# Kernel tuning notes

Hardware: AMD Instinct MI355X
Metric: run time of the kernel (lower is better)

The kernel has to match this reference:

```python
import jax, jax.numpy as jnp
import numpy as np

IN_DIM, H, OUT_DIM = 64, 128, 64
B, T = 1024, 512
NEG_SLOPE = 0.01
LN_EPS = 1e-5


def _mlp_layer(x, W, b, g, beta):
    h = x @ W.T + b
    h = jnp.where(h > 0, h, NEG_SLOPE * h)  # LeakyReLU
    mu = h.mean(-1, keepdims=True)
    var = h.var(-1, keepdims=True)
    return g * (h - mu) / jnp.sqrt(var + LN_EPS) + beta


def setup_inputs() -> dict:
    key = jax.random.key(0)
    ks = jax.random.split(key, 16)
    s = 1.0 / np.sqrt(H)
    return {
        "x": jax.random.normal(ks[0], (B, T, IN_DIM), jnp.float32),
        "is_init": jax.random.randint(ks[1], (B, T, 1), 0, 2) > 0,
        "hx": jax.random.normal(ks[2], (B, H), jnp.float32),
        "W1": jax.random.uniform(ks[3], (H, IN_DIM), jnp.float32, -s, s),
        "b1": jnp.zeros((H,), jnp.float32),
        "g1": jnp.ones((H,), jnp.float32),
        "beta1": jnp.zeros((H,), jnp.float32),
        "W2": jax.random.uniform(ks[4], (H, H), jnp.float32, -s, s),
        "b2": jnp.zeros((H,), jnp.float32),
        "g2": jnp.ones((H,), jnp.float32),
        "beta2": jnp.zeros((H,), jnp.float32),
        "W_ih": jax.random.uniform(ks[5], (3 * H, H), jnp.float32, -s, s),
        "W_hh": jax.random.uniform(ks[6], (3 * H, H), jnp.float32, -s, s),
        "b_ih": jax.random.uniform(ks[7], (3 * H,), jnp.float32, -s, s),
        "b_hh": jax.random.uniform(ks[8], (3 * H,), jnp.float32, -s, s),
        "W_out": jax.random.uniform(ks[9], (OUT_DIM, H), jnp.float32, -s, s),
        "b_out": jnp.zeros((OUT_DIM,), jnp.float32),
    }


def reference(x, is_init, hx, W1, b1, g1, beta1, W2, b2, g2, beta2,
              W_ih, W_hh, b_ih, b_hh, W_out, b_out):
    # MLP: two (Linear -> LeakyReLU -> LayerNorm) layers, width 128
    h = _mlp_layer(x, W1, b1, g1, beta1)
    h = _mlp_layer(h, W2, b2, g2, beta2)

    # Precompute input-side gate preactivations for all timesteps: [B,T,3H]
    gates_x = h @ W_ih.T + b_ih
    gates_x_t = jnp.swapaxes(gates_x, 0, 1)      # [T,B,3H]
    init_t = jnp.swapaxes(is_init, 0, 1)         # [T,B,1]

    def step(h_prev, inp):
        gx, init = inp
        h_prev = jnp.where(init, 0.0, h_prev)    # reset-on-init
        gh = h_prev @ W_hh.T + b_hh
        xr, xz, xn = jnp.split(gx, 3, axis=-1)
        hr, hz, hn = jnp.split(gh, 3, axis=-1)
        r = jax.nn.sigmoid(xr + hr)
        z = jax.nn.sigmoid(xz + hz)
        n = jnp.tanh(xn + r * hn)
        h_new = (1.0 - z) * n + z * h_prev
        return h_new, h_new

    hx_final, ys = jax.lax.scan(step, hx, (gates_x_t, init_t))
    y = jnp.swapaxes(ys, 0, 1)                   # [B,T,H]
    out = y @ W_out.T + b_out                    # [B,T,OUT_DIM]
    return out, hx_final
```

## Files before the change

kernel.cpp:

```cpp
#include <hip/hip_runtime.h>
#include <hip/hip_bf16.h>

#define IN_DIM 64
#define H 128
#define G3 384
#define OUT_DIM 64
#define Bb 1024
#define Tt 512
#define NEG 0.01f
#define EPSLN 1e-5f

#define CHUNK 16
#define NTILE (Tt / CHUNK)

typedef __bf16 bf16_t;
typedef __bf16 bf16x8 __attribute__((ext_vector_type(8)));
typedef float f32x4 __attribute__((ext_vector_type(4)));

#define MFMA(a, b, c) __builtin_amdgcn_mfma_f32_16x16x32_bf16((a), (b), (c), 0, 0, 0)

#define WS_W1 0
#define WS_W2 8192
#define WS_WIH 24576
#define WS_WHH 73728
#define WS_WOUT 122880
#define WS_ELEMS 131072
#define WS_E_OFF 262144
#define WS_R_OFF (WS_E_OFF + 16777216)
#define WS_RA_OFF (WS_R_OFF + 131072)
#define WS_NEED (WS_RA_OFF + 131072)

#define HAS 136
#define GXS 392

__global__ void cvt_weights(const float* __restrict__ W1, const float* __restrict__ W2,
                            const float* __restrict__ Wih, const float* __restrict__ Whh,
                            const float* __restrict__ Wout, bf16_t* __restrict__ ws,
                            int* __restrict__ RA) {
    int i = blockIdx.x * 256 + threadIdx.x;
    float v;
    if (i < WS_W2) v = W1[i];
    else if (i < WS_WIH) v = W2[i - WS_W2];
    else if (i < WS_WHH) v = Wih[i - WS_WIH];
    else if (i < WS_WOUT) v = Whh[i - WS_WHH];
    else v = Wout[i - WS_WOUT];
    ws[i] = (bf16_t)v;
    if (i < Bb * NTILE) RA[i] = 0;
}

#define P1_GX 0
#define P1_HA 50176
#define P1_HPB 67584
#define P1_RED 76288
#define P1_MNR 78336
#define P1_INI 78848
#define P1_SMEM 79120
#define BPB1 4

__global__ void __launch_bounds__(256, 2) gru_pass1(
    const float* __restrict__ x, const int* __restrict__ is_init,
    const float* __restrict__ hx,
    const float* __restrict__ b1, const float* __restrict__ g1, const float* __restrict__ be1,
    const float* __restrict__ b2, const float* __restrict__ g2, const float* __restrict__ be2,
    const float* __restrict__ bih, const float* __restrict__ bhh,
    const float* __restrict__ bout,
    const bf16_t* __restrict__ wsb,
    float* __restrict__ E, int* __restrict__ R,
    float* __restrict__ out)
{
    extern __shared__ char smem[];
    bf16_t* GX  = (bf16_t*)(smem + P1_GX);
    bf16_t* HA  = (bf16_t*)(smem + P1_HA);
    bf16_t* HPB = (bf16_t*)(smem + P1_HPB);
    float*  RED = (float*) (smem + P1_RED);
    float*  MNR = (float*) (smem + P1_MNR);
    int*    INI = (int*)   (smem + P1_INI);

    const bf16_t* W1B  = wsb + WS_W1;
    const bf16_t* W2B  = wsb + WS_W2;
    const bf16_t* WihB = wsb + WS_WIH;
    const bf16_t* WhhB = wsb + WS_WHH;
    const bf16_t* WoB  = wsb + WS_WOUT;

    const int tid  = threadIdx.x;
    const int w    = tid >> 6;
    const int lane = tid & 63;
    const int ln   = lane & 15;
    const int quad = lane >> 4;
    const int b0   = blockIdx.x * BPB1;
    const int tile = blockIdx.y;
    const int t0   = tile * CHUNK;

    for (int i = tid; i < 2 * 16 * HAS; i += 256) HPB[i] = (bf16_t)0.f;
    __syncthreads();

    float hp[2] = {0.f, 0.f};
    if (tile == 0) {
        const int b = quad;
        int im = is_init[(size_t)(b0 + b) * Tt];
#pragma unroll
        for (int sub = 0; sub < 2; ++sub) {
            int j = w * 32 + sub * 16 + ln;
            float v = im ? 0.f : hx[(size_t)(b0 + b) * H + j];
            hp[sub] = v;
            HPB[b * 4 * HAS + j] = (bf16_t)v;
        }
    }
    float bh[3][2];
#pragma unroll
    for (int g = 0; g < 3; ++g)
#pragma unroll
        for (int sub = 0; sub < 2; ++sub)
            bh[g][sub] = bhh[g * H + w * 32 + sub * 16 + ln];

    bf16x8 whhf[6][4];
#pragma unroll
    for (int ntl = 0; ntl < 6; ++ntl) {
        int gate = ntl >> 1, sub = ntl & 1;
        int n = gate * H + w * 32 + sub * 16 + ln;
#pragma unroll
        for (int ks = 0; ks < 4; ++ks)
            whhf[ntl][ks] = *(const bf16x8*)(WhhB + (size_t)n * H + ks * 32 + quad * 8);
    }
    __syncthreads();

    f32x4 vs[BPB1][2];

    {
        bf16x8 w1f[2][2];
#pragma unroll
        for (int ntl = 0; ntl < 2; ++ntl) {
            int n = w * 32 + ntl * 16 + ln;
#pragma unroll
            for (int ks = 0; ks < 2; ++ks)
                w1f[ntl][ks] = *(const bf16x8*)(W1B + (size_t)n * IN_DIM + ks * 32 + quad * 8);
        }
#pragma unroll
        for (int mt = 0; mt < BPB1; ++mt) {
            const float* xr_ = x + ((size_t)(b0 + mt) * Tt + t0 + ln) * IN_DIM;
            bf16x8 a0, a1;
#pragma unroll
            for (int j = 0; j < 8; ++j) {
                a0[j] = (bf16_t)xr_[quad * 8 + j];
                a1[j] = (bf16_t)xr_[32 + quad * 8 + j];
            }
#pragma unroll
            for (int ntl = 0; ntl < 2; ++ntl) {
                f32x4 c = {0.f, 0.f, 0.f, 0.f};
                c = MFMA(a0, w1f[ntl][0], c);
                c = MFMA(a1, w1f[ntl][1], c);
                vs[mt][ntl] = c;
            }
        }
        float bv[2], gv[2], bev[2];
#pragma unroll
        for (int ntl = 0; ntl < 2; ++ntl) {
            int n = w * 32 + ntl * 16 + ln;
            bv[ntl] = b1[n]; gv[ntl] = g1[n]; bev[ntl] = be1[n];
        }
#pragma unroll
        for (int mt = 0; mt < BPB1; ++mt) {
#pragma unroll
            for (int reg = 0; reg < 4; ++reg) {
                float v0 = vs[mt][0][reg] + bv[0]; v0 = v0 > 0.f ? v0 : NEG * v0;
                float v1 = vs[mt][1][reg] + bv[1]; v1 = v1 > 0.f ? v1 : NEG * v1;
                vs[mt][0][reg] = v0; vs[mt][1][reg] = v1;
                float s = v0 + v1, q = v0 * v0 + v1 * v1;
#pragma unroll
                for (int d = 1; d < 16; d <<= 1) { s += __shfl_xor(s, d); q += __shfl_xor(q, d); }
                if (ln == 0) {
                    int rr = mt * 16 + quad * 4 + reg;
                    RED[rr * 8 + w] = s; RED[rr * 8 + 4 + w] = q;
                }
            }
        }
        __syncthreads();
        if (tid < 64) {
            float s = RED[tid * 8] + RED[tid * 8 + 1] + RED[tid * 8 + 2] + RED[tid * 8 + 3];
            float q = RED[tid * 8 + 4] + RED[tid * 8 + 5] + RED[tid * 8 + 6] + RED[tid * 8 + 7];
            float mean = s * (1.f / H);
            float var = q * (1.f / H) - mean * mean;
            MNR[tid * 2] = mean; MNR[tid * 2 + 1] = rsqrtf(var + EPSLN);
        }
        __syncthreads();
#pragma unroll
        for (int mt = 0; mt < BPB1; ++mt) {
#pragma unroll
            for (int reg = 0; reg < 4; ++reg) {
                int rr = mt * 16 + quad * 4 + reg;
                float mean = MNR[rr * 2], rstd = MNR[rr * 2 + 1];
#pragma unroll
                for (int ntl = 0; ntl < 2; ++ntl) {
                    int n = w * 32 + ntl * 16 + ln;
                    HA[rr * HAS + n] = (bf16_t)(gv[ntl] * (vs[mt][ntl][reg] - mean) * rstd + bev[ntl]);
                }
            }
        }
        __syncthreads();
    }

    {
        bf16x8 w2f[2][4];
#pragma unroll
        for (int ntl = 0; ntl < 2; ++ntl) {
            int n = w * 32 + ntl * 16 + ln;
#pragma unroll
            for (int ks = 0; ks < 4; ++ks)
                w2f[ntl][ks] = *(const bf16x8*)(W2B + (size_t)n * H + ks * 32 + quad * 8);
        }
#pragma unroll
        for (int mt = 0; mt < BPB1; ++mt) {
            bf16x8 af[4];
#pragma unroll
            for (int ks = 0; ks < 4; ++ks)
                af[ks] = *(const bf16x8*)(HA + (mt * 16 + ln) * HAS + ks * 32 + quad * 8);
#pragma unroll
            for (int ntl = 0; ntl < 2; ++ntl) {
                f32x4 c = {0.f, 0.f, 0.f, 0.f};
#pragma unroll
                for (int ks = 0; ks < 4; ++ks) c = MFMA(af[ks], w2f[ntl][ks], c);
                vs[mt][ntl] = c;
            }
        }
        float bv[2], gv[2], bev[2];
#pragma unroll
        for (int ntl = 0; ntl < 2; ++ntl) {
            int n = w * 32 + ntl * 16 + ln;
            bv[ntl] = b2[n]; gv[ntl] = g2[n]; bev[ntl] = be2[n];
        }
#pragma unroll
        for (int mt = 0; mt < BPB1; ++mt) {
#pragma unroll
            for (int reg = 0; reg < 4; ++reg) {
                float v0 = vs[mt][0][reg] + bv[0]; v0 = v0 > 0.f ? v0 : NEG * v0;
                float v1 = vs[mt][1][reg] + bv[1]; v1 = v1 > 0.f ? v1 : NEG * v1;
                vs[mt][0][reg] = v0; vs[mt][1][reg] = v1;
                float s = v0 + v1, q = v0 * v0 + v1 * v1;
#pragma unroll
                for (int d = 1; d < 16; d <<= 1) { s += __shfl_xor(s, d); q += __shfl_xor(q, d); }
                if (ln == 0) {
                    int rr = mt * 16 + quad * 4 + reg;
                    RED[rr * 8 + w] = s; RED[rr * 8 + 4 + w] = q;
                }
            }
        }
        __syncthreads();
        if (tid < 64) {
            float s = RED[tid * 8] + RED[tid * 8 + 1] + RED[tid * 8 + 2] + RED[tid * 8 + 3];
            float q = RED[tid * 8 + 4] + RED[tid * 8 + 5] + RED[tid * 8 + 6] + RED[tid * 8 + 7];
            float mean = s * (1.f / H);
            float var = q * (1.f / H) - mean * mean;
            MNR[tid * 2] = mean; MNR[tid * 2 + 1] = rsqrtf(var + EPSLN);
        }
        __syncthreads();
#pragma unroll
        for (int mt = 0; mt < BPB1; ++mt) {
#pragma unroll
            for (int reg = 0; reg < 4; ++reg) {
                int rr = mt * 16 + quad * 4 + reg;
                float mean = MNR[rr * 2], rstd = MNR[rr * 2 + 1];
#pragma unroll
                for (int ntl = 0; ntl < 2; ++ntl) {
                    int n = w * 32 + ntl * 16 + ln;
                    HA[rr * HAS + n] = (bf16_t)(gv[ntl] * (vs[mt][ntl][reg] - mean) * rstd + bev[ntl]);
                }
            }
        }
        __syncthreads();
    }

#pragma unroll
    for (int half = 0; half < 2; ++half) {
        bf16x8 wf[3][4];
        float bv[3];
#pragma unroll
        for (int k3 = 0; k3 < 3; ++k3) {
            int n = (w * 6 + half * 3 + k3) * 16 + ln;
            bv[k3] = bih[n];
#pragma unroll
            for (int ks = 0; ks < 4; ++ks)
                wf[k3][ks] = *(const bf16x8*)(WihB + (size_t)n * H + ks * 32 + quad * 8);
        }
#pragma unroll
        for (int mt = 0; mt < BPB1; ++mt) {
            bf16x8 af[4];
#pragma unroll
            for (int ks = 0; ks < 4; ++ks)
                af[ks] = *(const bf16x8*)(HA + (mt * 16 + ln) * HAS + ks * 32 + quad * 8);
#pragma unroll
            for (int k3 = 0; k3 < 3; ++k3) {
                int n = (w * 6 + half * 3 + k3) * 16 + ln;
                f32x4 c = {0.f, 0.f, 0.f, 0.f};
#pragma unroll
                for (int ks = 0; ks < 4; ++ks) c = MFMA(af[ks], wf[k3][ks], c);
#pragma unroll
                for (int reg = 0; reg < 4; ++reg)
                    GX[(mt * 16 + quad * 4 + reg) * GXS + n] = (bf16_t)(c[reg] + bv[k3]);
            }
        }
    }
    if (tid < BPB1 * 17) {
        int b = tid / 17, s = tid % 17;
        int t = t0 + s;
        INI[tid] = (t < Tt) ? is_init[(size_t)(b0 + b) * Tt + t] : 0;
    }

    for (int s = 0; s < CHUNK; ++s) {
        __syncthreads();
        const int t = t0 + s;
        const int rp = t & 1;
        bf16x8 af[4];
#pragma unroll
        for (int ks = 0; ks < 4; ++ks)
            af[ks] = *(const bf16x8*)(HPB + rp * 16 * HAS + ln * HAS + ks * 32 + quad * 8);
        f32x4 gc[6];
#pragma unroll
        for (int ntl = 0; ntl < 6; ++ntl) {
            f32x4 c = {0.f, 0.f, 0.f, 0.f};
#pragma unroll
            for (int ks = 0; ks < 4; ++ks) c = MFMA(af[ks], whhf[ntl][ks], c);
            gc[ntl] = c;
        }
        {
            const int b = quad;
            bf16_t* hw = HPB + (rp ^ 1) * 16 * HAS + b * 4 * HAS;
            const int rbase = (b * 16 + s) * GXS;
#pragma unroll
            for (int sub = 0; sub < 2; ++sub) {
                int j = w * 32 + sub * 16 + ln;
                float xr = (float)GX[rbase + j];
                float xz = (float)GX[rbase + H + j];
                float xn = (float)GX[rbase + 2 * H + j];
                float hr = gc[sub][0]     + bh[0][sub];
                float hz = gc[2 + sub][0] + bh[1][sub];
                float hn = gc[4 + sub][0] + bh[2][sub];
                float r = 1.f / (1.f + __expf(-(xr + hr)));
                float z = 1.f / (1.f + __expf(-(xz + hz)));
                float a = xn + r * hn;
                a = fminf(fmaxf(a, -15.f), 15.f);
                float e = __expf(-2.f * a);
                float nn = (1.f - e) / (1.f + e);
                float hnew = (1.f - z) * nn + z * hp[sub];
                HA[(b * 16 + s) * HAS + j] = (bf16_t)hnew;
                float hm;
                if (s < CHUNK - 1) {
                    hm = INI[b * 17 + s + 1] ? 0.f : hnew;
                } else {
                    hm = hnew;
                    E[((size_t)(b0 + b) * NTILE + tile) * H + j] = hnew;
                }
                hp[sub] = hm;
                hw[j] = (bf16_t)hm;
            }
        }
    }
    __syncthreads();

    if (tid < BPB1) {
        int any = 0;
#pragma unroll
        for (int s = 0; s < CHUNK; ++s) any |= INI[tid * 17 + s];
        R[(b0 + tid) * NTILE + tile] = (tile == 0) ? 1 : (any ? 1 : 0);
    }

    {
        int o = w * 16 + ln;
        bf16x8 wof[4];
#pragma unroll
        for (int ks = 0; ks < 4; ++ks)
            wof[ks] = *(const bf16x8*)(WoB + (size_t)o * H + ks * 32 + quad * 8);
        float bo = bout[o];
#pragma unroll
        for (int mt = 0; mt < BPB1; ++mt) {
            bf16x8 af[4];
#pragma unroll
            for (int ks = 0; ks < 4; ++ks)
                af[ks] = *(const bf16x8*)(HA + (mt * 16 + ln) * HAS + ks * 32 + quad * 8);
            f32x4 c = {0.f, 0.f, 0.f, 0.f};
#pragma unroll
            for (int ks = 0; ks < 4; ++ks) c = MFMA(af[ks], wof[ks], c);
#pragma unroll
            for (int reg = 0; reg < 4; ++reg)
                out[((size_t)(b0 + mt) * Tt + t0 + quad * 4 + reg) * OUT_DIM + o] = c[reg] + bo;
        }
    }
}

__global__ void __launch_bounds__(256, 2) gru_fixp(
    const float* __restrict__ x, const int* __restrict__ is_init,
    const float* __restrict__ b1, const float* __restrict__ g1, const float* __restrict__ be1,
    const float* __restrict__ b2, const float* __restrict__ g2, const float* __restrict__ be2,
    const float* __restrict__ bih, const float* __restrict__ bhh,
    const float* __restrict__ bout,
    const bf16_t* __restrict__ wsb,
    float* __restrict__ E, const int* __restrict__ R, int* __restrict__ RA,
    float* __restrict__ out)
{
    __shared__ bf16_t sHA[16 * HAS];
    __shared__ bf16_t sHPB[2][16 * HAS];
    __shared__ float  sHPF[16 * 128];
    __shared__ float  sRED[16 * 8];
    __shared__ float  sMNR[16 * 2];
    __shared__ int    sINI[16 * 16];
    __shared__ int    sF[16];
    __shared__ int    sNeed[16];
    __shared__ int    sAny, sMaxf;

    const bf16_t* W1B  = wsb + WS_W1;
    const bf16_t* W2B  = wsb + WS_W2;
    const bf16_t* WihB = wsb + WS_WIH;
    const bf16_t* WhhB = wsb + WS_WHH;
    const bf16_t* WoB  = wsb + WS_WOUT;

    const int tid  = threadIdx.x;
    const int w    = tid >> 6;
    const int lane = tid & 63;
    const int ln   = lane & 15;
    const int quad = lane >> 4;
    const int bB   = blockIdx.x * 16;
    const int i    = blockIdx.y + 1;
    const int t0   = i * CHUNK;

    {
        int b = tid >> 4, s = tid & 15;
        sINI[tid] = is_init[(size_t)(bB + b) * Tt + t0 + s];
    }
    if (tid < 16) sNeed[tid] = R[(bB + tid) * NTILE + (i - 1)];
    if (tid == 0) { sAny = 0; sMaxf = 0; }
    __syncthreads();
    if (tid < 16) {
        int f = 16;
        for (int s = 15; s >= 0; --s) if (sINI[tid * 16 + s]) f = s;
        sF[tid] = f;
        int need = (sNeed[tid] && f > 0) ? 1 : 0;
        sNeed[tid] = need;
        if (need) { atomicOr(&sAny, 1); atomicMax(&sMaxf, f); }
    }
    __syncthreads();
    if (!sAny) return;
    const int maxf = sMaxf;

    for (int idx = tid; idx < 16 * 128; idx += 256) {
        int b = idx >> 7, j = idx & 127;
        float v = sNeed[b] ? E[((size_t)(bB + b) * NTILE + i - 1) * H + j] : 0.f;
        sHPF[idx] = v;
        sHPB[0][b * HAS + j] = (bf16_t)v;
        sHPB[1][b * HAS + j] = (bf16_t)0.f;
    }

    float bh[3][2], bihv[6];
#pragma unroll
    for (int g = 0; g < 3; ++g)
#pragma unroll
        for (int sub = 0; sub < 2; ++sub) {
            int j = w * 32 + sub * 16 + ln;
            bh[g][sub] = bhh[g * H + j];
            bihv[g * 2 + sub] = bih[g * H + j];
        }
    float bv1[2], gv1[2], bev1[2], bv2[2], gv2[2], bev2[2];
#pragma unroll
    for (int ntl = 0; ntl < 2; ++ntl) {
        int n = w * 32 + ntl * 16 + ln;
        bv1[ntl] = b1[n]; gv1[ntl] = g1[n]; bev1[ntl] = be1[n];
        bv2[ntl] = b2[n]; gv2[ntl] = g2[n]; bev2[ntl] = be2[n];
    }
    bf16x8 whhf[6][4];
#pragma unroll
    for (int ntl = 0; ntl < 6; ++ntl) {
        int gate = ntl >> 1, sub = ntl & 1;
        int n = gate * H + w * 32 + sub * 16 + ln;
#pragma unroll
        for (int ks = 0; ks < 4; ++ks)
            whhf[ntl][ks] = *(const bf16x8*)(WhhB + (size_t)n * H + ks * 32 + quad * 8);
    }
    bf16x8 wof[4];
    {
        int o = w * 16 + ln;
#pragma unroll
        for (int ks = 0; ks < 4; ++ks)
            wof[ks] = *(const bf16x8*)(WoB + (size_t)o * H + ks * 32 + quad * 8);
    }
    float bo = bout[w * 16 + ln];
    __syncthreads();

    for (int s = 0; s < maxf; ++s) {
        const int t = t0 + s;
        const int par = s & 1;
        f32x4 vs[2];

        {
            const float* xr_ = x + ((size_t)(bB + ln) * Tt + t) * IN_DIM;
            bf16x8 a0, a1;
#pragma unroll
            for (int j = 0; j < 8; ++j) {
                a0[j] = (bf16_t)xr_[quad * 8 + j];
                a1[j] = (bf16_t)xr_[32 + quad * 8 + j];
            }
#pragma unroll
            for (int ntl = 0; ntl < 2; ++ntl) {
                int n = w * 32 + ntl * 16 + ln;
                bf16x8 f0 = *(const bf16x8*)(W1B + (size_t)n * IN_DIM + quad * 8);
                bf16x8 f1 = *(const bf16x8*)(W1B + (size_t)n * IN_DIM + 32 + quad * 8);
                f32x4 c = {0.f, 0.f, 0.f, 0.f};
                c = MFMA(a0, f0, c);
                c = MFMA(a1, f1, c);
                vs[ntl] = c;
            }
        }
#pragma unroll
        for (int reg = 0; reg < 4; ++reg) {
            float v0 = vs[0][reg] + bv1[0]; v0 = v0 > 0.f ? v0 : NEG * v0;
            float v1 = vs[1][reg] + bv1[1]; v1 = v1 > 0.f ? v1 : NEG * v1;
            vs[0][reg] = v0; vs[1][reg] = v1;
            float sm = v0 + v1, q = v0 * v0 + v1 * v1;
#pragma unroll
            for (int d = 1; d < 16; d <<= 1) { sm += __shfl_xor(sm, d); q += __shfl_xor(q, d); }
            if (ln == 0) {
                int rr = quad * 4 + reg;
                sRED[rr * 8 + w] = sm; sRED[rr * 8 + 4 + w] = q;
            }
        }
        __syncthreads();
        if (tid < 16) {
            float sm = sRED[tid * 8] + sRED[tid * 8 + 1] + sRED[tid * 8 + 2] + sRED[tid * 8 + 3];
            float q = sRED[tid * 8 + 4] + sRED[tid * 8 + 5] + sRED[tid * 8 + 6] + sRED[tid * 8 + 7];
            float mean = sm * (1.f / H);
            float var = q * (1.f / H) - mean * mean;
            sMNR[tid * 2] = mean; sMNR[tid * 2 + 1] = rsqrtf(var + EPSLN);
        }
        __syncthreads();
#pragma unroll
        for (int reg = 0; reg < 4; ++reg) {
            int rr = quad * 4 + reg;
            float mean = sMNR[rr * 2], rstd = sMNR[rr * 2 + 1];
#pragma unroll
            for (int ntl = 0; ntl < 2; ++ntl) {
                int n = w * 32 + ntl * 16 + ln;
                sHA[rr * HAS + n] = (bf16_t)(gv1[ntl] * (vs[ntl][reg] - mean) * rstd + bev1[ntl]);
            }
        }
        __syncthreads();

        {
            bf16x8 af[4];
#pragma unroll
            for (int ks = 0; ks < 4; ++ks)
                af[ks] = *(const bf16x8*)(sHA + ln * HAS + ks * 32 + quad * 8);
#pragma unroll
            for (int ntl = 0; ntl < 2; ++ntl) {
                int n = w * 32 + ntl * 16 + ln;
                f32x4 c = {0.f, 0.f, 0.f, 0.f};
#pragma unroll
                for (int ks = 0; ks < 4; ++ks) {
                    bf16x8 f = *(const bf16x8*)(W2B + (size_t)n * H + ks * 32 + quad * 8);
                    c = MFMA(af[ks], f, c);
                }
                vs[ntl] = c;
            }
        }
        __syncthreads();
#pragma unroll
        for (int reg = 0; reg < 4; ++reg) {
            float v0 = vs[0][reg] + bv2[0]; v0 = v0 > 0.f ? v0 : NEG * v0;
            float v1 = vs[1][reg] + bv2[1]; v1 = v1 > 0.f ? v1 : NEG * v1;
            vs[0][reg] = v0; vs[1][reg] = v1;
            float sm = v0 + v1, q = v0 * v0 + v1 * v1;
#pragma unroll
            for (int d = 1; d < 16; d <<= 1) { sm += __shfl_xor(sm, d); q += __shfl_xor(q, d); }
            if (ln == 0) {
                int rr = quad * 4 + reg;
                sRED[rr * 8 + w] = sm; sRED[rr * 8 + 4 + w] = q;
            }
        }
        __syncthreads();
        if (tid < 16) {
            float sm = sRED[tid * 8] + sRED[tid * 8 + 1] + sRED[tid * 8 + 2] + sRED[tid * 8 + 3];
            float q = sRED[tid * 8 + 4] + sRED[tid * 8 + 5] + sRED[tid * 8 + 6] + sRED[tid * 8 + 7];
            float mean = sm * (1.f / H);
            float var = q * (1.f / H) - mean * mean;
            sMNR[tid * 2] = mean; sMNR[tid * 2 + 1] = rsqrtf(var + EPSLN);
        }
        __syncthreads();
#pragma unroll
        for (int reg = 0; reg < 4; ++reg) {
            int rr = quad * 4 + reg;
            float mean = sMNR[rr * 2], rstd = sMNR[rr * 2 + 1];
#pragma unroll
            for (int ntl = 0; ntl < 2; ++ntl) {
                int n = w * 32 + ntl * 16 + ln;
                sHA[rr * HAS + n] = (bf16_t)(gv2[ntl] * (vs[ntl][reg] - mean) * rstd + bev2[ntl]);
            }
        }
        __syncthreads();

        bf16x8 af2[4], afh[4];
#pragma unroll
        for (int ks = 0; ks < 4; ++ks) {
            af2[ks] = *(const bf16x8*)(sHA + ln * HAS + ks * 32 + quad * 8);
            afh[ks] = *(const bf16x8*)(sHPB[par] + ln * HAS + ks * 32 + quad * 8);
        }
        f32x4 gxc[6], ghc[6];
#pragma unroll
        for (int ntl = 0; ntl < 6; ++ntl) {
            int gate = ntl >> 1, sub = ntl & 1;
            int n = gate * H + w * 32 + sub * 16 + ln;
            f32x4 cg = {0.f, 0.f, 0.f, 0.f};
#pragma unroll
            for (int ks = 0; ks < 4; ++ks) {
                bf16x8 f = *(const bf16x8*)(WihB + (size_t)n * H + ks * 32 + quad * 8);
                cg = MFMA(af2[ks], f, cg);
            }
            gxc[ntl] = cg;
            f32x4 ch = {0.f, 0.f, 0.f, 0.f};
#pragma unroll
            for (int ks = 0; ks < 4; ++ks) ch = MFMA(afh[ks], whhf[ntl][ks], ch);
            ghc[ntl] = ch;
        }
        __syncthreads();

#pragma unroll
        for (int reg = 0; reg < 4; ++reg) {
            const int b = quad * 4 + reg;
            const int msk = sNeed[b] && (s < sF[b]);
#pragma unroll
            for (int sub = 0; sub < 2; ++sub) {
                int j = w * 32 + sub * 16 + ln;
                float xr = gxc[sub][reg]     + bihv[sub];
                float xz = gxc[2 + sub][reg] + bihv[2 + sub];
                float xn = gxc[4 + sub][reg] + bihv[4 + sub];
                float hr = ghc[sub][reg]     + bh[0][sub];
                float hz = ghc[2 + sub][reg] + bh[1][sub];
                float hn = ghc[4 + sub][reg] + bh[2][sub];
                float r = 1.f / (1.f + __expf(-(xr + hr)));
                float z = 1.f / (1.f + __expf(-(xz + hz)));
                float a = xn + r * hn;
                a = fminf(fmaxf(a, -15.f), 15.f);
                float e = __expf(-2.f * a);
                float nn = (1.f - e) / (1.f + e);
                float hp = sHPF[b * 128 + j];
                float hnew = (1.f - z) * nn + z * hp;
                if (msk) {
                    sHPF[b * 128 + j] = hnew;
                    sHPB[par ^ 1][b * HAS + j] = (bf16_t)hnew;
                    sHA[b * HAS + j] = (bf16_t)hnew;
                }
            }
        }
        __syncthreads();

        {
            bf16x8 af[4];
#pragma unroll
            for (int ks = 0; ks < 4; ++ks)
                af[ks] = *(const bf16x8*)(sHA + ln * HAS + ks * 32 + quad * 8);
            f32x4 c = {0.f, 0.f, 0.f, 0.f};
#pragma unroll
            for (int ks = 0; ks < 4; ++ks) c = MFMA(af[ks], wof[ks], c);
            int o = w * 16 + ln;
#pragma unroll
            for (int reg = 0; reg < 4; ++reg) {
                int b = quad * 4 + reg;
                if (sNeed[b] && s < sF[b])
                    out[((size_t)(bB + b) * Tt + t) * OUT_DIM + o] = c[reg] + bo;
            }
        }
        __syncthreads();
    }

    for (int idx = tid; idx < 16 * 128; idx += 256) {
        int b = idx >> 7, j = idx & 127;
        if (sNeed[b] && sF[b] == 16)
            E[((size_t)(bB + b) * NTILE + i) * H + j] = sHPF[b * 128 + j];
    }
    if (tid < 16 && sNeed[tid] && sF[tid] == 16)
        RA[(bB + tid) * NTILE + i] = 1;
}

__global__ void __launch_bounds__(128) gru_sweep(
    const float* __restrict__ x, const int* __restrict__ is_init,
    const float* __restrict__ W1, const float* __restrict__ b1,
    const float* __restrict__ g1, const float* __restrict__ be1,
    const float* __restrict__ W2, const float* __restrict__ b2,
    const float* __restrict__ g2, const float* __restrict__ be2,
    const float* __restrict__ Wih, const float* __restrict__ Whh,
    const float* __restrict__ bih, const float* __restrict__ bhh,
    const float* __restrict__ Wout, const float* __restrict__ bout,
    const float* __restrict__ E, const int* __restrict__ R, const int* __restrict__ RA,
    float* __restrict__ out)
{
    __shared__ float sX[64], sH1[128], sH2[128], sHH[128], sRS[4];
    __shared__ int sI[16], sFf;

    const int b = blockIdx.x;
    const int j = threadIdx.x;
    const int wv = j >> 6, lj = j & 63;

    float h = E[((size_t)b * NTILE) * H + j];

    for (int i = 1; i < NTILE; ++i) {
        int Rm1 = R[b * NTILE + i - 1];
        if (!Rm1) {
            if (j < 16) sI[j] = is_init[(size_t)b * Tt + i * CHUNK + j];
            __syncthreads();
            if (j == 0) {
                int f = 16;
                for (int s = 15; s >= 0; --s) if (sI[s]) f = s;
                sFf = f;
            }
            __syncthreads();
            int f = sFf;
            for (int s = 0; s < f; ++s) {
                int t = i * CHUNK + s;
                sHH[j] = h;
                if (j < 64) sX[j] = x[((size_t)b * Tt + t) * IN_DIM + j];
                __syncthreads();
                float a1 = b1[j];
                const float* w1r = W1 + (size_t)j * IN_DIM;
                for (int k = 0; k < 64; ++k) a1 += sX[k] * w1r[k];
                a1 = a1 > 0.f ? a1 : NEG * a1;
                {
                    float sv = a1, sq = a1 * a1;
                    for (int d = 1; d < 64; d <<= 1) { sv += __shfl_xor(sv, d); sq += __shfl_xor(sq, d); }
                    if (lj == 0) { sRS[wv * 2] = sv; sRS[wv * 2 + 1] = sq; }
                    __syncthreads();
                    float mean = (sRS[0] + sRS[2]) * (1.f / H);
                    float var = (sRS[1] + sRS[3]) * (1.f / H) - mean * mean;
                    a1 = g1[j] * (a1 - mean) * rsqrtf(var + EPSLN) + be1[j];
                }
                sH1[j] = a1;
                __syncthreads();
                float a2 = b2[j];
                const float* w2r = W2 + (size_t)j * H;
                for (int k = 0; k < 128; ++k) a2 += sH1[k] * w2r[k];
                a2 = a2 > 0.f ? a2 : NEG * a2;
                {
                    float sv = a2, sq = a2 * a2;
                    for (int d = 1; d < 64; d <<= 1) { sv += __shfl_xor(sv, d); sq += __shfl_xor(sq, d); }
                    if (lj == 0) { sRS[wv * 2] = sv; sRS[wv * 2 + 1] = sq; }
                    __syncthreads();
                    float mean = (sRS[0] + sRS[2]) * (1.f / H);
                    float var = (sRS[1] + sRS[3]) * (1.f / H) - mean * mean;
                    a2 = g2[j] * (a2 - mean) * rsqrtf(var + EPSLN) + be2[j];
                }
                sH2[j] = a2;
                __syncthreads();
                float gx0 = bih[j], gx1 = bih[H + j], gx2 = bih[2 * H + j];
                float gh0 = bhh[j], gh1 = bhh[H + j], gh2 = bhh[2 * H + j];
                const float* wi0 = Wih + (size_t)j * H;
                const float* wi1 = Wih + (size_t)(H + j) * H;
                const float* wi2 = Wih + (size_t)(2 * H + j) * H;
                const float* wh0 = Whh + (size_t)j * H;
                const float* wh1 = Whh + (size_t)(H + j) * H;
                const float* wh2 = Whh + (size_t)(2 * H + j) * H;
                for (int k = 0; k < 128; ++k) {
                    float h2k = sH2[k], hhk = sHH[k];
                    gx0 += h2k * wi0[k]; gx1 += h2k * wi1[k]; gx2 += h2k * wi2[k];
                    gh0 += hhk * wh0[k]; gh1 += hhk * wh1[k]; gh2 += hhk * wh2[k];
                }
                float r = 1.f / (1.f + __expf(-(gx0 + gh0)));
                float z = 1.f / (1.f + __expf(-(gx1 + gh1)));
                float a = gx2 + r * gh2;
                a = fminf(fmaxf(a, -15.f), 15.f);
                float e = __expf(-2.f * a);
                float nn = (1.f - e) / (1.f + e);
                h = (1.f - z) * nn + z * h;
                __syncthreads();
                sH1[j] = h;
                __syncthreads();
                if (j < 64) {
                    float o = bout[j];
                    const float* wo = Wout + (size_t)j * H;
                    for (int k = 0; k < 128; ++k) o += sH1[k] * wo[k];
                    out[((size_t)b * Tt + t) * OUT_DIM + j] = o;
                }
                __syncthreads();
            }
            if (f < 16) h = E[((size_t)b * NTILE + i) * H + j];
        } else {
            if (R[b * NTILE + i] || RA[b * NTILE + i])
                h = E[((size_t)b * NTILE + i) * H + j];
        }
    }
    out[(size_t)Bb * Tt * OUT_DIM + (size_t)b * H + j] = h;
}

#define FGX_OFF 0
#define FHA_OFF 25088
#define FHPB_OFF 33792
#define FRED_OFF 42496
#define FMNR_OFF 43520
#define FVEC_OFF 43776
#define FINI_OFF 50176
#define FSMEM 50320
#define FV_B1 0
#define FV_G1 128
#define FV_BE1 256
#define FV_B2 384
#define FV_G2 512
#define FV_BE2 640
#define FV_BIH 768
#define FV_BHH 1152
#define FV_BOUT 1536

__global__ void __launch_bounds__(256, 2) gru_seq(
    const float* __restrict__ x, const int* __restrict__ is_init,
    const float* __restrict__ hx,
    const float* __restrict__ W1, const float* __restrict__ b1,
    const float* __restrict__ g1, const float* __restrict__ be1,
    const float* __restrict__ W2, const float* __restrict__ b2,
    const float* __restrict__ g2, const float* __restrict__ be2,
    const float* __restrict__ Wih, const float* __restrict__ Whh,
// ... 219 lines not shown
                }
            }
            __syncthreads();
        }
#pragma unroll
        for (int half = 0; half < 2; ++half) {
            bf16x8 wf[3][4];
            float bv[3];
#pragma unroll
            for (int k3 = 0; k3 < 3; ++k3) {
                int n = (w * 6 + half * 3 + k3) * 16 + ln;
                bv[k3] = VEC[FV_BIH + n];
                const float* p = Wih + (size_t)n * H;
#pragma unroll
                for (int ks = 0; ks < 4; ++ks) {
                    const float* q = p + ks * 32 + quad * 8;
                    bf16x8 f;
#pragma unroll
                    for (int jj = 0; jj < 8; ++jj) f[jj] = (bf16_t)q[jj];
                    wf[k3][ks] = f;
                }
            }
#pragma unroll
            for (int mt = 0; mt < 2; ++mt) {
                bf16x8 af[4];
#pragma unroll
                for (int ks = 0; ks < 4; ++ks)
                    af[ks] = *(const bf16x8*)(HA + (mt * 16 + ln) * HAS + ks * 32 + quad * 8);
#pragma unroll
                for (int k3 = 0; k3 < 3; ++k3) {
                    int n = (w * 6 + half * 3 + k3) * 16 + ln;
                    f32x4 c = {0.f, 0.f, 0.f, 0.f};
#pragma unroll
                    for (int ks = 0; ks < 4; ++ks) c = MFMA(af[ks], wf[k3][ks], c);
#pragma unroll
                    for (int reg = 0; reg < 4; ++reg)
                        GX[(mt * 16 + quad * 4 + reg) * GXS + n] = (bf16_t)(c[reg] + bv[k3]);
                }
            }
        }
        if (tid < 2 * 17) {
            int b = tid / 17, s = tid % 17;
            int t = t0 + s;
            INI[tid] = (t < Tt) ? is_init[(size_t)(b0 + b) * Tt + t] : 0;
        }
        for (int s = 0; s < CHUNK; ++s) {
            __syncthreads();
            const int t = t0 + s;
            const int rp = t & 1;
            bf16x8 af[4];
#pragma unroll
            for (int ks = 0; ks < 4; ++ks)
                af[ks] = *(const bf16x8*)(HPB + rp * 16 * HAS + ln * HAS + ks * 32 + quad * 8);
            f32x4 gc[6];
#pragma unroll
            for (int ntl = 0; ntl < 6; ++ntl) {
                f32x4 c = {0.f, 0.f, 0.f, 0.f};
#pragma unroll
                for (int ks = 0; ks < 4; ++ks) c = MFMA(af[ks], whhf[ntl][ks], c);
                gc[ntl] = c;
            }
            if (quad < 2) {
                const int b = quad;
                bf16_t* hw = HPB + (rp ^ 1) * 16 * HAS + b * 4 * HAS;
                const int rbase = (b * 16 + s) * GXS;
#pragma unroll
                for (int sub = 0; sub < 2; ++sub) {
                    int jj = w * 32 + sub * 16 + ln;
                    float xr = (float)GX[rbase + jj];
                    float xz = (float)GX[rbase + H + jj];
                    float xn = (float)GX[rbase + 2 * H + jj];
                    float hr = gc[sub][0]     + bh[0][sub];
                    float hz = gc[2 + sub][0] + bh[1][sub];
                    float hn = gc[4 + sub][0] + bh[2][sub];
                    float r = 1.f / (1.f + __expf(-(xr + hr)));
                    float z = 1.f / (1.f + __expf(-(xz + hz)));
                    float a = xn + r * hn;
                    a = fminf(fmaxf(a, -15.f), 15.f);
                    float e = __expf(-2.f * a);
                    float nn = (1.f - e) / (1.f + e);
                    float hnew = (1.f - z) * nn + z * hp[sub];
                    HA[(b * 16 + s) * HAS + jj] = (bf16_t)hnew;
                    float hm;
                    if (t < Tt - 1) {
                        hm = INI[b * 17 + s + 1] ? 0.f : hnew;
                    } else {
                        hm = hnew;
                        out[(size_t)Bb * Tt * OUT_DIM + (size_t)(b0 + b) * H + jj] = hnew;
                    }
                    hp[sub] = hm;
                    hw[jj] = (bf16_t)hm;
                }
            }
        }
        __syncthreads();
        {
            int o = w * 16 + ln;
            const float* p = Wout + (size_t)o * H;
            bf16x8 wof[4];
#pragma unroll
            for (int ks = 0; ks < 4; ++ks) {
                const float* q = p + ks * 32 + quad * 8;
                bf16x8 f;
#pragma unroll
                for (int jj = 0; jj < 8; ++jj) f[jj] = (bf16_t)q[jj];
                wof[ks] = f;
            }
            float bo = VEC[FV_BOUT + o];
#pragma unroll
            for (int mt = 0; mt < 2; ++mt) {
                bf16x8 af[4];
#pragma unroll
                for (int ks = 0; ks < 4; ++ks)
                    af[ks] = *(const bf16x8*)(HA + (mt * 16 + ln) * HAS + ks * 32 + quad * 8);
                f32x4 c = {0.f, 0.f, 0.f, 0.f};
#pragma unroll
                for (int ks = 0; ks < 4; ++ks) c = MFMA(af[ks], wof[ks], c);
#pragma unroll
                for (int reg = 0; reg < 4; ++reg)
                    out[((size_t)(b0 + mt) * Tt + t0 + quad * 4 + reg) * OUT_DIM + o] = c[reg] + bo;
            }
        }
        __syncthreads();
    }
}

extern "C" void kernel_launch(void* const* d_in, const int* in_sizes, int n_in,
                              void* d_out, int out_size, void* d_ws, size_t ws_size,
                              hipStream_t stream) {
    const float* x      = (const float*)d_in[0];
    const int*   is_init= (const int*)  d_in[1];
    const float* hx     = (const float*)d_in[2];
    const float* W1     = (const float*)d_in[3];
    const float* b1     = (const float*)d_in[4];
    const float* g1     = (const float*)d_in[5];
    const float* be1    = (const float*)d_in[6];
    const float* W2     = (const float*)d_in[7];
    const float* b2     = (const float*)d_in[8];
    const float* g2     = (const float*)d_in[9];
    const float* be2    = (const float*)d_in[10];
    const float* Wih    = (const float*)d_in[11];
    const float* Whh    = (const float*)d_in[12];
    const float* bih    = (const float*)d_in[13];
    const float* bhh    = (const float*)d_in[14];
    const float* Wout   = (const float*)d_in[15];
    const float* bout   = (const float*)d_in[16];
    float* out = (float*)d_out;

    if (d_ws != nullptr && ws_size >= (size_t)WS_NEED) {
        bf16_t* wsb = (bf16_t*)d_ws;
        float*  E   = (float*)((char*)d_ws + WS_E_OFF);
        int*    R   = (int*)  ((char*)d_ws + WS_R_OFF);
        int*    RA  = (int*)  ((char*)d_ws + WS_RA_OFF);

        cvt_weights<<<WS_ELEMS / 256, 256, 0, stream>>>(W1, W2, Wih, Whh, Wout, wsb, RA);

        hipFuncSetAttribute((const void*)gru_pass1,
                            hipFuncAttributeMaxDynamicSharedMemorySize, P1_SMEM);
        gru_pass1<<<dim3(Bb / BPB1, NTILE), 256, P1_SMEM, stream>>>(
            x, is_init, hx, b1, g1, be1, b2, g2, be2, bih, bhh, bout,
            wsb, E, R, out);

        gru_fixp<<<dim3(Bb / 16, NTILE - 1), 256, 0, stream>>>(
            x, is_init, b1, g1, be1, b2, g2, be2, bih, bhh, bout,
            wsb, E, R, RA, out);

        gru_sweep<<<Bb, 128, 0, stream>>>(
            x, is_init, W1, b1, g1, be1, W2, b2, g2, be2,
            Wih, Whh, bih, bhh, Wout, bout, E, R, RA, out);
    } else {
        hipFuncSetAttribute((const void*)gru_seq,
                            hipFuncAttributeMaxDynamicSharedMemorySize, FSMEM);
        gru_seq<<<Bb / 2, 256, FSMEM, stream>>>(
            x, is_init, hx, W1, b1, g1, be1, W2, b2, g2, be2,
            Wih, Whh, bih, bhh, Wout, bout, out);
    }
}
```

Baseline: 1.346 ms.

## Cut pass1 shared memory, pre-convert x to bf16, drop fixp weight registers

Adds a kernel that converts x to bf16 once in workspace, so pass1 and fixp load x with vector bf16 loads instead of scalar fp32 loads plus conversion. Pass1 now computes input-gate preactivations in two halves of 8 timesteps and packs the hidden-state double buffer into a single tile, which halves the GX buffer and shrinks LDS enough to raise launch bounds to 3 blocks per CU. The fixp kernel stops holding the Whh and Wout fragments in registers and reloads them from global memory per step, lowering register pressure at the cost of extra memory traffic. The x conversion adds a separate pass over the 128MB input and requires a larger workspace, falling back to the old path otherwise.

```diff
diff --git a/kernel.cpp b/kernel.cpp
--- a/kernel.cpp
+++ b/kernel.cpp
@@ -14,6 +14,7 @@
 #define NTILE (Tt / CHUNK)
 
 typedef __bf16 bf16_t;
+typedef __bf16 bf16x4 __attribute__((ext_vector_type(4)));
 typedef __bf16 bf16x8 __attribute__((ext_vector_type(8)));
 typedef float f32x4 __attribute__((ext_vector_type(4)));
 
@@ -29,6 +30,8 @@
 #define WS_R_OFF (WS_E_OFF + 16777216)
 #define WS_RA_OFF (WS_R_OFF + 131072)
 #define WS_NEED (WS_RA_OFF + 131072)
+#define WS_XB_OFF WS_NEED
+#define WS_XB_NEED (WS_XB_OFF + 67108864)
 
 #define HAS 136
 #define GXS 392
@@ -48,18 +51,27 @@
     if (i < Bb * NTILE) RA[i] = 0;
 }
 
+__global__ void cvt_x(const float* __restrict__ x, bf16_t* __restrict__ xb) {
+    size_t i = ((size_t)blockIdx.x * 256 + threadIdx.x) * 4;
+    float4 v = *(const float4*)(x + i);
+    bf16x4 o;
+    o[0] = (bf16_t)v.x; o[1] = (bf16_t)v.y; o[2] = (bf16_t)v.z; o[3] = (bf16_t)v.w;
+    *(bf16x4*)(xb + i) = o;
+}
+
 #define P1_GX 0
-#define P1_HA 50176
-#define P1_HPB 67584
-#define P1_RED 76288
-#define P1_MNR 78336
-#define P1_INI 78848
-#define P1_SMEM 79120
+#define P1_HA 25088
+#define P1_HPB 42496
+#define P1_RED 46848
+#define P1_MNR 48896
+#define P1_INI 49408
+#define P1_SMEM 49680
 #define BPB1 4
 
-__global__ void __launch_bounds__(256, 2) gru_pass1(
-    const float* __restrict__ x, const int* __restrict__ is_init,
-    const float* __restrict__ hx,
+template <bool XBF>
+__global__ void __launch_bounds__(256, 3) gru_pass1(
+    const float* __restrict__ x, const bf16_t* __restrict__ xb,
+    const int* __restrict__ is_init, const float* __restrict__ hx,
     const float* __restrict__ b1, const float* __restrict__ g1, const float* __restrict__ be1,
     const float* __restrict__ b2, const float* __restrict__ g2, const float* __restrict__ be2,
     const float* __restrict__ bih, const float* __restrict__ bhh,
@@ -91,7 +103,7 @@
     const int tile = blockIdx.y;
     const int t0   = tile * CHUNK;
 
-    for (int i = tid; i < 2 * 16 * HAS; i += 256) HPB[i] = (bf16_t)0.f;
+    for (int i = tid; i < 16 * HAS; i += 256) HPB[i] = (bf16_t)0.f;
     __syncthreads();
 
     float hp[2] = {0.f, 0.f};
@@ -137,12 +149,18 @@
         }
 #pragma unroll
         for (int mt = 0; mt < BPB1; ++mt) {
-            const float* xr_ = x + ((size_t)(b0 + mt) * Tt + t0 + ln) * IN_DIM;
             bf16x8 a0, a1;
-#pragma unroll
-            for (int j = 0; j < 8; ++j) {
-                a0[j] = (bf16_t)xr_[quad * 8 + j];
-                a1[j] = (bf16_t)xr_[32 + quad * 8 + j];
+            if constexpr (XBF) {
+                const bf16_t* xr_ = xb + ((size_t)(b0 + mt) * Tt + t0 + ln) * IN_DIM;
+                a0 = *(const bf16x8*)(xr_ + quad * 8);
+                a1 = *(const bf16x8*)(xr_ + 32 + quad * 8);
+            } else {
+                const float* xr_ = x + ((size_t)(b0 + mt) * Tt + t0 + ln) * IN_DIM;
+#pragma unroll
+                for (int j = 0; j < 8; ++j) {
+                    a0[j] = (bf16_t)xr_[quad * 8 + j];
+                    a1[j] = (bf16_t)xr_[32 + quad * 8 + j];
+                }
             }
 #pragma unroll
             for (int ntl = 0; ntl < 2; ++ntl) {
@@ -269,88 +287,93 @@
         __syncthreads();
     }
 
-#pragma unroll
-    for (int half = 0; half < 2; ++half) {
-        bf16x8 wf[3][4];
-        float bv[3];
-#pragma unroll
-        for (int k3 = 0; k3 < 3; ++k3) {
-            int n = (w * 6 + half * 3 + k3) * 16 + ln;
-            bv[k3] = bih[n];
-#pragma unroll
-            for (int ks = 0; ks < 4; ++ks)
-                wf[k3][ks] = *(const bf16x8*)(WihB + (size_t)n * H + ks * 32 + quad * 8);
-        }
-#pragma unroll
-        for (int mt = 0; mt < BPB1; ++mt) {
-            bf16x8 af[4];
-#pragma unroll
-            for (int ks = 0; ks < 4; ++ks)
-                af[ks] = *(const bf16x8*)(HA + (mt * 16 + ln) * HAS + ks * 32 + quad * 8);
-#pragma unroll
-            for (int k3 = 0; k3 < 3; ++k3) {
-                int n = (w * 6 + half * 3 + k3) * 16 + ln;
-                f32x4 c = {0.f, 0.f, 0.f, 0.f};
-#pragma unroll
-                for (int ks = 0; ks < 4; ++ks) c = MFMA(af[ks], wf[k3][ks], c);
-#pragma unroll
-                for (int reg = 0; reg < 4; ++reg)
-                    GX[(mt * 16 + quad * 4 + reg) * GXS + n] = (bf16_t)(c[reg] + bv[k3]);
-            }
-        }
-    }
     if (tid < BPB1 * 17) {
         int b = tid / 17, s = tid % 17;
         int t = t0 + s;
         INI[tid] = (t < Tt) ? is_init[(size_t)(b0 + b) * Tt + t] : 0;
     }
 
-    for (int s = 0; s < CHUNK; ++s) {
-        __syncthreads();
-        const int t = t0 + s;
-        const int rp = t & 1;
-        bf16x8 af[4];
-#pragma unroll
-        for (int ks = 0; ks < 4; ++ks)
-            af[ks] = *(const bf16x8*)(HPB + rp * 16 * HAS + ln * HAS + ks * 32 + quad * 8);
-        f32x4 gc[6];
-#pragma unroll
-        for (int ntl = 0; ntl < 6; ++ntl) {
-            f32x4 c = {0.f, 0.f, 0.f, 0.f};
-#pragma unroll
-            for (int ks = 0; ks < 4; ++ks) c = MFMA(af[ks], whhf[ntl][ks], c);
-            gc[ntl] = c;
-        }
-        {
-            const int b = quad;
-            bf16_t* hw = HPB + (rp ^ 1) * 16 * HAS + b * 4 * HAS;
-            const int rbase = (b * 16 + s) * GXS;
-#pragma unroll
-            for (int sub = 0; sub < 2; ++sub) {
-                int j = w * 32 + sub * 16 + ln;
-                float xr = (float)GX[rbase + j];
-                float xz = (float)GX[rbase + H + j];
-                float xn = (float)GX[rbase + 2 * H + j];
-                float hr = gc[sub][0]     + bh[0][sub];
-                float hz = gc[2 + sub][0] + bh[1][sub];
-                float hn = gc[4 + sub][0] + bh[2][sub];
-                float r = 1.f / (1.f + __expf(-(xr + hr)));
-                float z = 1.f / (1.f + __expf(-(xz + hz)));
-                float a = xn + r * hn;
-                a = fminf(fmaxf(a, -15.f), 15.f);
-                float e = __expf(-2.f * a);
-                float nn = (1.f - e) / (1.f + e);
-                float hnew = (1.f - z) * nn + z * hp[sub];
-                HA[(b * 16 + s) * HAS + j] = (bf16_t)hnew;
-                float hm;
-                if (s < CHUNK - 1) {
-                    hm = INI[b * 17 + s + 1] ? 0.f : hnew;
-                } else {
-                    hm = hnew;
-                    E[((size_t)(b0 + b) * NTILE + tile) * H + j] = hnew;
-                }
-                hp[sub] = hm;
-                hw[j] = (bf16_t)hm;
+#pragma unroll 1
+    for (int hf = 0; hf < 2; ++hf) {
+        if (hf == 1) __syncthreads();
+#pragma unroll
+        for (int half3 = 0; half3 < 2; ++half3) {
+            bf16x8 wf[3][4];
+            float bv[3];
+#pragma unroll
+            for (int k3 = 0; k3 < 3; ++k3) {
+                int n = (w * 6 + half3 * 3 + k3) * 16 + ln;
+                bv[k3] = bih[n];
+#pragma unroll
+                for (int ks = 0; ks < 4; ++ks)
+                    wf[k3][ks] = *(const bf16x8*)(WihB + (size_t)n * H + ks * 32 + quad * 8);
+            }
+#pragma unroll
+            for (int mt2 = 0; mt2 < 2; ++mt2) {
+                bf16x8 af[4];
+                int arow = (mt2 * 2 + (ln >> 3)) * 16 + hf * 8 + (ln & 7);
+#pragma unroll
+                for (int ks = 0; ks < 4; ++ks)
+                    af[ks] = *(const bf16x8*)(HA + arow * HAS + ks * 32 + quad * 8);
+                int grow = (mt2 * 2 + (quad >> 1)) * 8 + (quad & 1) * 4;
+#pragma unroll
+                for (int k3 = 0; k3 < 3; ++k3) {
+                    int n = (w * 6 + half3 * 3 + k3) * 16 + ln;
+                    f32x4 c = {0.f, 0.f, 0.f, 0.f};
+#pragma unroll
+                    for (int ks = 0; ks < 4; ++ks) c = MFMA(af[ks], wf[k3][ks], c);
+#pragma unroll
+                    for (int reg = 0; reg < 4; ++reg)
+                        GX[(grow + reg) * GXS + n] = (bf16_t)(c[reg] + bv[k3]);
+                }
+            }
+        }
+
+        for (int s = hf * 8; s < hf * 8 + 8; ++s) {
+            __syncthreads();
+            const int rp = s & 1;
+            bf16x8 af[4];
+#pragma unroll
+            for (int ks = 0; ks < 4; ++ks)
+                af[ks] = *(const bf16x8*)(HPB + ln * HAS + ks * 32 + quad * 8);
+            f32x4 gc[6];
+#pragma unroll
+            for (int ntl = 0; ntl < 6; ++ntl) {
+                f32x4 c = {0.f, 0.f, 0.f, 0.f};
+#pragma unroll
+                for (int ks = 0; ks < 4; ++ks) c = MFMA(af[ks], whhf[ntl][ks], c);
+                gc[ntl] = c;
+            }
+            {
+                const int b = quad;
+                const int gxrow = (b * 8 + (s & 7)) * GXS;
+#pragma unroll
+                for (int sub = 0; sub < 2; ++sub) {
+                    int j = w * 32 + sub * 16 + ln;
+                    float xr = (float)GX[gxrow + j];
+                    float xz = (float)GX[gxrow + H + j];
+                    float xn = (float)GX[gxrow + 2 * H + j];
+                    float hr = gc[sub][rp]     + bh[0][sub];
+                    float hz = gc[2 + sub][rp] + bh[1][sub];
+                    float hn = gc[4 + sub][rp] + bh[2][sub];
+                    float r = 1.f / (1.f + __expf(-(xr + hr)));
+                    float z = 1.f / (1.f + __expf(-(xz + hz)));
+                    float a = xn + r * hn;
+                    a = fminf(fmaxf(a, -15.f), 15.f);
+                    float e = __expf(-2.f * a);
+                    float nn = (1.f - e) / (1.f + e);
+                    float hnew = (1.f - z) * nn + z * hp[sub];
+                    HA[(b * 16 + s) * HAS + j] = (bf16_t)hnew;
+                    float hm;
+                    if (s < CHUNK - 1) {
+                        hm = INI[b * 17 + s + 1] ? 0.f : hnew;
+                    } else {
+                        hm = hnew;
+                        E[((size_t)(b0 + b) * NTILE + tile) * H + j] = hnew;
+                    }
+                    hp[sub] = hm;
+                    HPB[(b * 4 + (rp ^ 1)) * HAS + j] = (bf16_t)hm;
+                }
             }
         }
     }
@@ -386,8 +409,10 @@
     }
 }
 
+template <bool XBF>
 __global__ void __launch_bounds__(256, 2) gru_fixp(
-    const float* __restrict__ x, const int* __restrict__ is_init,
+    const float* __restrict__ x, const bf16_t* __restrict__ xb,
+    const int* __restrict__ is_init,
     const float* __restrict__ b1, const float* __restrict__ g1, const float* __restrict__ be1,
     const float* __restrict__ b2, const float* __restrict__ g2, const float* __restrict__ be2,
     const float* __restrict__ bih, const float* __restrict__ bhh,
@@ -464,22 +489,6 @@
         bv1[ntl] = b1[n]; gv1[ntl] = g1[n]; bev1[ntl] = be1[n];
         bv2[ntl] = b2[n]; gv2[ntl] = g2[n]; bev2[ntl] = be2[n];
     }
-    bf16x8 whhf[6][4];
-#pragma unroll
-    for (int ntl = 0; ntl < 6; ++ntl) {
-        int gate = ntl >> 1, sub = ntl & 1;
-        int n = gate * H + w * 32 + sub * 16 + ln;
-#pragma unroll
-        for (int ks = 0; ks < 4; ++ks)
-            whhf[ntl][ks] = *(const bf16x8*)(WhhB + (size_t)n * H + ks * 32 + quad * 8);
-    }
-    bf16x8 wof[4];
-    {
-        int o = w * 16 + ln;
-#pragma unroll
-        for (int ks = 0; ks < 4; ++ks)
-            wof[ks] = *(const bf16x8*)(WoB + (size_t)o * H + ks * 32 + quad * 8);
-    }
     float bo = bout[w * 16 + ln];
     __syncthreads();
 
@@ -489,12 +498,18 @@
         f32x4 vs[2];
 
         {
-            const float* xr_ = x + ((size_t)(bB + ln) * Tt + t) * IN_DIM;
             bf16x8 a0, a1;
-#pragma unroll
-            for (int j = 0; j < 8; ++j) {
-                a0[j] = (bf16_t)xr_[quad * 8 + j];
-                a1[j] = (bf16_t)xr_[32 + quad * 8 + j];
+            if constexpr (XBF) {
+                const bf16_t* xr_ = xb + ((size_t)(bB + ln) * Tt + t) * IN_DIM;
+                a0 = *(const bf16x8*)(xr_ + quad * 8);
+                a1 = *(const bf16x8*)(xr_ + 32 + quad * 8);
+            } else {
+                const float* xr_ = x + ((size_t)(bB + ln) * Tt + t) * IN_DIM;
+#pragma unroll
+                for (int j = 0; j < 8; ++j) {
+                    a0[j] = (bf16_t)xr_[quad * 8 + j];
+                    a1[j] = (bf16_t)xr_[32 + quad * 8 + j];
+                }
             }
 #pragma unroll
             for (int ntl = 0; ntl < 2; ++ntl) {
@@ -605,15 +620,15 @@
             int gate = ntl >> 1, sub = ntl & 1;
             int n = gate * H + w * 32 + sub * 16 + ln;
             f32x4 cg = {0.f, 0.f, 0.f, 0.f};
+            f32x4 ch = {0.f, 0.f, 0.f, 0.f};
 #pragma unroll
             for (int ks = 0; ks < 4; ++ks) {
-                bf16x8 f = *(const bf16x8*)(WihB + (size_t)n * H + ks * 32 + quad * 8);
-                cg = MFMA(af2[ks], f, cg);
+                bf16x8 fi = *(const bf16x8*)(WihB + (size_t)n * H + ks * 32 + quad * 8);
+                bf16x8 fh = *(const bf16x8*)(WhhB + (size_t)n * H + ks * 32 + quad * 8);
+                cg = MFMA(af2[ks], fi, cg);
+                ch = MFMA(afh[ks], fh, ch);
             }
             gxc[ntl] = cg;
-            f32x4 ch = {0.f, 0.f, 0.f, 0.f};
-#pragma unroll
-            for (int ks = 0; ks < 4; ++ks) ch = MFMA(afh[ks], whhf[ntl][ks], ch);
             ghc[ntl] = ch;
         }
         __syncthreads();
@@ -653,10 +668,13 @@
 #pragma unroll
             for (int ks = 0; ks < 4; ++ks)
                 af[ks] = *(const bf16x8*)(sHA + ln * HAS + ks * 32 + quad * 8);
+            int o = w * 16 + ln;
             f32x4 c = {0.f, 0.f, 0.f, 0.f};
 #pragma unroll
-            for (int ks = 0; ks < 4; ++ks) c = MFMA(af[ks], wof[ks], c);
-            int o = w * 16 + ln;
+            for (int ks = 0; ks < 4; ++ks) {
+                bf16x8 fo = *(const bf16x8*)(WoB + (size_t)o * H + ks * 32 + quad * 8);
+                c = MFMA(af[ks], fo, c);
+            }
 #pragma unroll
             for (int reg = 0; reg < 4; ++reg) {
                 int b = quad * 4 + reg;
@@ -1182,18 +1200,31 @@
         float*  E   = (float*)((char*)d_ws + WS_E_OFF);
         int*    R   = (int*)  ((char*)d_ws + WS_R_OFF);
         int*    RA  = (int*)  ((char*)d_ws + WS_RA_OFF);
+        const bool xbf = ws_size >= (size_t)WS_XB_NEED;
+        bf16_t* xb = xbf ? (bf16_t*)((char*)d_ws + WS_XB_OFF) : nullptr;
 
         cvt_weights<<<WS_ELEMS / 256, 256, 0, stream>>>(W1, W2, Wih, Whh, Wout, wsb, RA);
 
-        hipFuncSetAttribute((const void*)gru_pass1,
-                            hipFuncAttributeMaxDynamicSharedMemorySize, P1_SMEM);
-        gru_pass1<<<dim3(Bb / BPB1, NTILE), 256, P1_SMEM, stream>>>(
-            x, is_init, hx, b1, g1, be1, b2, g2, be2, bih, bhh, bout,
-            wsb, E, R, out);
-
-        gru_fixp<<<dim3(Bb / 16, NTILE - 1), 256, 0, stream>>>(
-            x, is_init, b1, g1, be1, b2, g2, be2, bih, bhh, bout,
-            wsb, E, R, RA, out);
+        if (xbf) {
+            cvt_x<<<(Bb * Tt * IN_DIM) / (256 * 4), 256, 0, stream>>>(x, xb);
+            hipFuncSetAttribute((const void*)gru_pass1<true>,
+                                hipFuncAttributeMaxDynamicSharedMemorySize, P1_SMEM);
+            gru_pass1<true><<<dim3(Bb / BPB1, NTILE), 256, P1_SMEM, stream>>>(
+                x, xb, is_init, hx, b1, g1, be1, b2, g2, be2, bih, bhh, bout,
+                wsb, E, R, out);
+            gru_fixp<true><<<dim3(Bb / 16, NTILE - 1), 256, 0, stream>>>(
+                x, xb, is_init, b1, g1, be1, b2, g2, be2, bih, bhh, bout,
+                wsb, E, R, RA, out);
+        } else {
+            hipFuncSetAttribute((const void*)gru_pass1<false>,
+                                hipFuncAttributeMaxDynamicSharedMemorySize, P1_SMEM);
+            gru_pass1<false><<<dim3(Bb / BPB1, NTILE), 256, P1_SMEM, stream>>>(
+                x, nullptr, is_init, hx, b1, g1, be1, b2, g2, be2, bih, bhh, bout,
+                wsb, E, R, out);
+            gru_fixp<false><<<dim3(Bb / 16, NTILE - 1), 256, 0, stream>>>(
+                x, nullptr, is_init, b1, g1, be1, b2, g2, be2, bih, bhh, bout,
+                wsb, E, R, RA, out);
+        }
 
         gru_sweep<<<Bb, 128, 0, stream>>>(
             x, is_init, W1, b1, g1, be1, W2, b2, g2, be2,
```

New measurement: 1.683 ms. 1.25x slower.
